# Kernel optimization log

Measured on AMD Instinct MI355X. Metric: run time of the kernel, lower is better.

The kernel has to match this reference:

```python
import jax, jax.numpy as jnp
import numpy as np
from jax import lax

NPOINT = 1024   # FPS centroids
NSAMPLE = 32    # neighbors per ball
RADIUS = 0.1    # ball-query radius (points live in unit cube)


def farthest_point_sample(pos, npoint):
    # pos: [B, N, 3] -> idx [B, npoint] int32
    B, N, _ = pos.shape

    def step(carry, _):
        min_d, far = carry                                   # [B,N], [B]
        centroid = jnp.take_along_axis(pos, far[:, None, None], axis=1)  # [B,1,3]
        d = jnp.sum((pos - centroid) ** 2, axis=-1)          # [B,N]
        min_d = jnp.minimum(min_d, d)
        nxt = jnp.argmax(min_d, axis=1).astype(jnp.int32)
        return (min_d, nxt), far

    init = (jnp.full((B, N), 1e10, pos.dtype), jnp.zeros((B,), jnp.int32))
    _, idx = lax.scan(step, init, None, length=npoint)
    return idx.T                                             # [B, npoint]


def ball_query(new_pos, pos, radius, k):
    # new_pos: [B,M,3], pos: [B,N,3] -> idx [B,M,k] int32
    d2 = (jnp.sum(new_pos ** 2, -1)[:, :, None]
          + jnp.sum(pos ** 2, -1)[:, None, :]
          - 2.0 * jnp.einsum('bmc,bnc->bmn', new_pos, pos))  # [B,M,N]
    neg = jnp.where(d2 <= radius * radius, -d2, -jnp.inf)
    vals, idx = lax.top_k(neg, k)                            # k nearest inside ball
    valid = vals > -jnp.inf
    idx = jnp.where(valid, idx, idx[..., :1])                # replicate first hit (centroid itself)
    return idx.astype(jnp.int32)


def setup_inputs() -> dict:
    key = jax.random.key(0)
    ks = jax.random.split(key, 6)
    B, N, C = 4, 16384, 1
    pos = jax.random.uniform(ks[0], (B, N, 3), dtype=jnp.float32)
    x = jax.random.normal(ks[1], (B, N, C), dtype=jnp.float32)
    c_in = 3 + C  # rel-xyz concat features
    W1 = jax.random.normal(ks[2], (c_in, 32), jnp.float32) * np.sqrt(2.0 / c_in)
    W2 = jax.random.normal(ks[3], (32, 32), jnp.float32) * np.sqrt(2.0 / 32)
    W3 = jax.random.normal(ks[4], (32, 32), jnp.float32) * np.sqrt(2.0 / 32)
    b1 = jnp.zeros((32,), jnp.float32)
    b2 = jnp.zeros((32,), jnp.float32)
    b3 = jnp.zeros((32,), jnp.float32)
    return {"pos": pos, "x": x, "W1": W1, "b1": b1, "W2": W2, "b2": b2, "W3": W3, "b3": b3}


def reference(pos, x, W1, b1, W2, b2, W3, b3):
    # PointNet++ set-abstraction: FPS -> ball query -> group -> shared MLP -> max-pool.
    fps_idx = farthest_point_sample(lax.stop_gradient(pos), NPOINT)       # [B,M]
    new_pos = jnp.take_along_axis(pos, fps_idx[..., None], axis=1)        # [B,M,3]
    idx = ball_query(lax.stop_gradient(new_pos), lax.stop_gradient(pos), RADIUS, NSAMPLE)  # [B,M,K]
    B, M, K = idx.shape
    flat = idx.reshape(B, M * K)
    gpos = jnp.take_along_axis(pos, flat[..., None], axis=1).reshape(B, M, K, 3)
    gx = jnp.take_along_axis(x, flat[..., None], axis=1).reshape(B, M, K, -1)
    rel = gpos - new_pos[:, :, None, :]                                   # local coords
    h = jnp.concatenate([rel, gx], axis=-1)                               # [B,M,K,4]
    h = jax.nn.relu(h @ W1 + b1)
    h = jax.nn.relu(h @ W2 + b2)
    h = jax.nn.relu(h @ W3 + b3)
    return jnp.max(h, axis=2)                                             # [B,M,32]
```

## Files before the change

kernel.cpp:

```cpp
#include <hip/hip_runtime.h>

#define NB 4
#define NPT 16384
#define NPOINT 1024
#define NSAMPLE 32

#define FPS_T 512
#define FPS_PPT (NPT / FPS_T)

#define BQ_WAVES 4
#define CAP 896

__global__ __launch_bounds__(FPS_T, 2) void fps_kernel(
    const float* __restrict__ pos, float* __restrict__ new_pos) {
#pragma clang fp contract(off)
  const int b = blockIdx.x;
  const int tid = threadIdx.x;
  const int wid = tid >> 6;
  const int lane = tid & 63;
  const float* __restrict__ p = pos + (size_t)b * NPT * 3;

  __shared__ float2 sxy[NPT];
  __shared__ unsigned long long red[3];

  float z[FPS_PPT], md[FPS_PPT];

  {
    const float4* pf4 = (const float4*)(p + (size_t)tid * (FPS_PPT * 3));
#pragma unroll
    for (int k = 0; k < FPS_PPT / 4; ++k) {
      const float4 a = pf4[3 * k + 0];
      const float4 bq = pf4[3 * k + 1];
      const float4 c = pf4[3 * k + 2];
      sxy[(4 * k + 0) * FPS_T + tid] = make_float2(a.x, a.y);
      z[4 * k + 0] = a.z;
      sxy[(4 * k + 1) * FPS_T + tid] = make_float2(a.w, bq.x);
      z[4 * k + 1] = bq.y;
      sxy[(4 * k + 2) * FPS_T + tid] = make_float2(bq.z, bq.w);
      z[4 * k + 2] = c.x;
      sxy[(4 * k + 3) * FPS_T + tid] = make_float2(c.y, c.z);
      z[4 * k + 3] = c.w;
    }
#pragma unroll
    for (int i = 0; i < FPS_PPT; ++i) md[i] = 1e10f;
  }

  if (tid < 3) red[tid] = 0ull;
  __syncthreads();

  float cx = p[0], cy = p[1], cz = p[2];

  for (int j = 0; j < NPOINT; ++j) {
    if (tid == 0) {
      float* q = new_pos + ((size_t)b * NPOINT + j) * 3;
      q[0] = cx;
      q[1] = cy;
      q[2] = cz;
    }
    float bm = -1.0f;
    int bi = 0;
#pragma unroll
    for (int i = 0; i < FPS_PPT; ++i) {
      const float2 xy = sxy[i * FPS_T + tid];
      const float dx = xy.x - cx;
      const float dy = xy.y - cy;
      const float dz = z[i] - cz;
      const float d = (dx * dx + dy * dy) + dz * dz;
      const float m = fminf(md[i], d);
      md[i] = m;
      if (m > bm) {
        bm = m;
        bi = i;
      }
    }
    float wm = bm;
#pragma unroll
    for (int off = 1; off < 64; off <<= 1)
      wm = fmaxf(wm, __shfl_xor(wm, off, 64));
    const unsigned long long tied = __ballot(bm == wm);
    const int wl = __ffsll((long long)tied) - 1;
    const int wbi = __shfl(bi, wl, 64);
    const int widx = ((wid << 6) + wl) * FPS_PPT + wbi;
    if (lane == 0) {
      const unsigned long long key =
          ((unsigned long long)__float_as_uint(wm) << 32) |
          (unsigned)(~widx);
      atomicMax(&red[j % 3], key);
    }
    __syncthreads();
    const unsigned long long w = red[j % 3];
    if (tid == 0) red[(j + 2) % 3] = 0ull;
    const int nf = (int)(~(unsigned)w);
    cx = p[nf * 3 + 0];
    cy = p[nf * 3 + 1];
    cz = p[nf * 3 + 2];
  }
}

__global__ __launch_bounds__(256) void bq_mlp_kernel(
    const float* __restrict__ pos, const float* __restrict__ x,
    const float* __restrict__ W1, const float* __restrict__ b1,
    const float* __restrict__ W2, const float* __restrict__ b2,
    const float* __restrict__ W3, const float* __restrict__ b3,
    const float* __restrict__ new_pos, float* __restrict__ out) {
#pragma clang fp contract(off)
  __shared__ __align__(16) float w1s[4 * 32];
  __shared__ __align__(16) float w2s[32 * 32];
  __shared__ __align__(16) float w3s[32 * 32];
  __shared__ float b1s[32], b2s[32], b3s[32];
  __shared__ unsigned long long list[BQ_WAVES][CAP];
  __shared__ int sel[BQ_WAVES][NSAMPLE];
  __shared__ unsigned cnt[BQ_WAVES];

  const int tid = threadIdx.x;
  const int wid = tid >> 6;
  const int lane = tid & 63;

  for (int i = tid; i < 128; i += 256) w1s[i] = W1[i];
  for (int i = tid; i < 1024; i += 256) {
    w2s[i] = W2[i];
    w3s[i] = W3[i];
  }
  if (tid < 32) {
    b1s[tid] = b1[tid];
    b2s[tid] = b2[tid];
    b3s[tid] = b3[tid];
  }
  if (lane == 0) cnt[wid] = 0u;
  __syncthreads();

  const int m_global = blockIdx.x * BQ_WAVES + wid;
  const int b = m_global >> 10;
  const float* __restrict__ p = pos + (size_t)b * NPT * 3;
  const float* __restrict__ xb = x + (size_t)b * NPT;

  const float cx = new_pos[(size_t)m_global * 3 + 0];
  const float cy = new_pos[(size_t)m_global * 3 + 1];
  const float cz = new_pos[(size_t)m_global * 3 + 2];
  const float snew = (cx * cx + cy * cy) + cz * cz;

  for (int it = 0; it < NPT / 256; ++it) {
    const int n0 = it * 256 + lane * 4;
    const float4* pf4 = (const float4*)(p + (size_t)n0 * 3);
    const float4 a = pf4[0];
    const float4 bq = pf4[1];
    const float4 c = pf4[2];
    float qx[4], qy[4], qz[4];
    qx[0] = a.x;  qy[0] = a.y;  qz[0] = a.z;
    qx[1] = a.w;  qy[1] = bq.x; qz[1] = bq.y;
    qx[2] = bq.z; qy[2] = bq.w; qz[2] = c.x;
    qx[3] = c.y;  qy[3] = c.z;  qz[3] = c.w;
#pragma unroll
    for (int t = 0; t < 4; ++t) {
      const float spos = (qx[t] * qx[t] + qy[t] * qy[t]) + qz[t] * qz[t];
      const float dot = (cx * qx[t] + cy * qy[t]) + cz * qz[t];
      const float d2 = (snew + spos) - 2.0f * dot;
      if (d2 <= 0.01f) {
        const unsigned u = __float_as_uint(d2);
        const unsigned key = (u & 0x80000000u) ? ~u : (u | 0x80000000u);
        const unsigned li = atomicAdd(&cnt[wid], 1u);
        if (li < CAP)
          list[wid][li] = ((unsigned long long)key << 32) | (unsigned)(n0 + t);
      }
    }
  }
  __syncthreads();

  int c = (int)cnt[wid];
  if (c > CAP) c = CAP;
  const int nsel = c < NSAMPLE ? c : NSAMPLE;

  for (int i = lane; i < c; i += 64) {
    const unsigned long long ki = list[wid][i];
    int rank = 0;
    for (int jj = 0; jj < c; ++jj) rank += (list[wid][jj] < ki) ? 1 : 0;
    if (rank < NSAMPLE) sel[wid][rank] = (int)(unsigned)(ki & 0xFFFFFFFFull);
  }
  __syncthreads();

  const bool active = (lane < nsel);
  const int n = sel[wid][active ? lane : 0];

  const float gpx = p[n * 3 + 0];
  const float gpy = p[n * 3 + 1];
  const float gpz = p[n * 3 + 2];
  const float gxv = xb[n];

  const float h0 = gpx - cx, h1i = gpy - cy, h2i = gpz - cz, h3i = gxv;

  float h1[32];
#pragma unroll
  for (int o = 0; o < 32; ++o) {
    float a = b1s[o];
    a += h0 * w1s[0 * 32 + o];
    a += h1i * w1s[1 * 32 + o];
    a += h2i * w1s[2 * 32 + o];
    a += h3i * w1s[3 * 32 + o];
    h1[o] = fmaxf(a, 0.0f);
  }

  float acc[32];
#pragma unroll
  for (int o = 0; o < 32; ++o) acc[o] = b2s[o];
  for (int k = 0; k < 32; ++k) {
    const float hk = h1[k];
    const float4* row = (const float4*)&w2s[k * 32];
#pragma unroll
    for (int q = 0; q < 8; ++q) {
      const float4 ww = row[q];
      acc[4 * q + 0] += hk * ww.x;
      acc[4 * q + 1] += hk * ww.y;
      acc[4 * q + 2] += hk * ww.z;
      acc[4 * q + 3] += hk * ww.w;
    }
  }
#pragma unroll
  for (int o = 0; o < 32; ++o) h1[o] = fmaxf(acc[o], 0.0f);

#pragma unroll
  for (int o = 0; o < 32; ++o) acc[o] = b3s[o];
  for (int k = 0; k < 32; ++k) {
    const float hk = h1[k];
    const float4* row = (const float4*)&w3s[k * 32];
#pragma unroll
    for (int q = 0; q < 8; ++q) {
      const float4 ww = row[q];
      acc[4 * q + 0] += hk * ww.x;
      acc[4 * q + 1] += hk * ww.y;
      acc[4 * q + 2] += hk * ww.z;
      acc[4 * q + 3] += hk * ww.w;
    }
  }
#pragma unroll
  for (int o = 0; o < 32; ++o)
    acc[o] = active ? fmaxf(acc[o], 0.0f) : -INFINITY;

#pragma unroll
  for (int mask = 1; mask <= 16; mask <<= 1) {
#pragma unroll
    for (int o = 0; o < 32; ++o)
      acc[o] = fmaxf(acc[o], __shfl_xor(acc[o], mask, 64));
  }

  if (lane == 0) {
    float4* o4 = (float4*)(out + (size_t)m_global * 32);
#pragma unroll
    for (int q = 0; q < 8; ++q)
      o4[q] = make_float4(acc[4 * q + 0], acc[4 * q + 1], acc[4 * q + 2],
                          acc[4 * q + 3]);
  }
}

extern "C" void kernel_launch(void* const* d_in, const int* in_sizes, int n_in,
                              void* d_out, int out_size, void* d_ws,
                              size_t ws_size, hipStream_t stream) {
  const float* pos = (const float*)d_in[0];
  const float* x = (const float*)d_in[1];
  const float* W1 = (const float*)d_in[2];
  const float* b1 = (const float*)d_in[3];
  const float* W2 = (const float*)d_in[4];
  const float* b2 = (const float*)d_in[5];
  const float* W3 = (const float*)d_in[6];
  const float* b3 = (const float*)d_in[7];
  float* out = (float*)d_out;
  float* new_pos = (float*)d_ws;

  fps_kernel<<<NB, FPS_T, 0, stream>>>(pos, new_pos);
  bq_mlp_kernel<<<(NB * NPOINT) / BQ_WAVES, 256, 0, stream>>>(
      pos, x, W1, b1, W2, b2, W3, b3, new_pos, out);
}
```

Measured before the change: 1.940 ms.

## Speed up FPS loop with DPP reduction, float4 LDS, and on-chip centroid fetch

The FPS inner loop now reads xy pairs for two points per LDS load by packing them into float4. The wave max uses DPP row/broadcast steps plus readlane instead of a shfl_xor butterfly. The next centroid is read from LDS, with z taken from a per-wave winner slot, instead of a dependent global load after the barrier. The new_pos write is also rotated across threads so it no longer always lands on thread 0. All of this shortens the serial per-iteration critical path, at the cost of relying on the index encoding and on DPP semantics being correct.

Measured after the change: 1.939 ms. Within noise of the previous version (-0.0%).

```diff
diff --git a/kernel.cpp b/kernel.cpp
--- a/kernel.cpp
+++ b/kernel.cpp
@@ -10,6 +10,13 @@
 
 #define BQ_WAVES 4
 #define CAP 896
+
+template <int CTRL>
+__device__ __forceinline__ float dpp_max_step(float v) {
+  const int s =
+      __builtin_amdgcn_update_dpp(0, __float_as_int(v), CTRL, 0xf, 0xf, true);
+  return fmaxf(v, __int_as_float(s));
+}
 
 __global__ __launch_bounds__(FPS_T, 2) void fps_kernel(
     const float* __restrict__ pos, float* __restrict__ new_pos) {
@@ -20,8 +27,9 @@
   const int lane = tid & 63;
   const float* __restrict__ p = pos + (size_t)b * NPT * 3;
 
-  __shared__ float2 sxy[NPT];
+  __shared__ float4 sxy4[NPT / 2];
   __shared__ unsigned long long red[3];
+  __shared__ float wzs[3][8];
 
   float z[FPS_PPT], md[FPS_PPT];
 
@@ -32,13 +40,11 @@
       const float4 a = pf4[3 * k + 0];
       const float4 bq = pf4[3 * k + 1];
       const float4 c = pf4[3 * k + 2];
-      sxy[(4 * k + 0) * FPS_T + tid] = make_float2(a.x, a.y);
+      sxy4[(2 * k + 0) * FPS_T + tid] = make_float4(a.x, a.y, a.w, bq.x);
+      sxy4[(2 * k + 1) * FPS_T + tid] = make_float4(bq.z, bq.w, c.y, c.z);
       z[4 * k + 0] = a.z;
-      sxy[(4 * k + 1) * FPS_T + tid] = make_float2(a.w, bq.x);
       z[4 * k + 1] = bq.y;
-      sxy[(4 * k + 2) * FPS_T + tid] = make_float2(bq.z, bq.w);
       z[4 * k + 2] = c.x;
-      sxy[(4 * k + 3) * FPS_T + tid] = make_float2(c.y, c.z);
       z[4 * k + 3] = c.w;
     }
 #pragma unroll
@@ -51,7 +57,7 @@
   float cx = p[0], cy = p[1], cz = p[2];
 
   for (int j = 0; j < NPOINT; ++j) {
-    if (tid == 0) {
+    if (tid == (((j & 7) << 6) | ((j >> 3) & 63))) {
       float* q = new_pos + ((size_t)b * NPOINT + j) * 3;
       q[0] = cx;
       q[1] = cy;
@@ -59,41 +65,71 @@
     }
     float bm = -1.0f;
     int bi = 0;
-#pragma unroll
-    for (int i = 0; i < FPS_PPT; ++i) {
-      const float2 xy = sxy[i * FPS_T + tid];
-      const float dx = xy.x - cx;
-      const float dy = xy.y - cy;
-      const float dz = z[i] - cz;
-      const float d = (dx * dx + dy * dy) + dz * dz;
-      const float m = fminf(md[i], d);
-      md[i] = m;
-      if (m > bm) {
-        bm = m;
-        bi = i;
+    float bz = 0.0f;
+#pragma unroll
+    for (int i2 = 0; i2 < FPS_PPT / 2; ++i2) {
+      const float4 q4 = sxy4[i2 * FPS_T + tid];
+      {
+        const int i = 2 * i2;
+        const float dx = q4.x - cx;
+        const float dy = q4.y - cy;
+        const float dz = z[i] - cz;
+        const float d = (dx * dx + dy * dy) + dz * dz;
+        const float m = fminf(md[i], d);
+        md[i] = m;
+        if (m > bm) {
+          bm = m;
+          bi = i;
+          bz = z[i];
+        }
       }
-    }
-    float wm = bm;
-#pragma unroll
-    for (int off = 1; off < 64; off <<= 1)
-      wm = fmaxf(wm, __shfl_xor(wm, off, 64));
+      {
+        const int i = 2 * i2 + 1;
+        const float dx = q4.z - cx;
+        const float dy = q4.w - cy;
+        const float dz = z[i] - cz;
+        const float d = (dx * dx + dy * dy) + dz * dz;
+        const float m = fminf(md[i], d);
+        md[i] = m;
+        if (m > bm) {
+          bm = m;
+          bi = i;
+          bz = z[i];
+        }
+      }
+    }
+    float v = bm;
+    v = dpp_max_step<0x111>(v);
+    v = dpp_max_step<0x112>(v);
+    v = dpp_max_step<0x114>(v);
+    v = dpp_max_step<0x118>(v);
+    v = dpp_max_step<0x142>(v);
+    v = dpp_max_step<0x143>(v);
+    const float wm =
+        __int_as_float(__builtin_amdgcn_readlane(__float_as_int(v), 63));
     const unsigned long long tied = __ballot(bm == wm);
     const int wl = __ffsll((long long)tied) - 1;
-    const int wbi = __shfl(bi, wl, 64);
+    const int wbi = __builtin_amdgcn_readlane(bi, wl);
+    const float wbz =
+        __int_as_float(__builtin_amdgcn_readlane(__float_as_int(bz), wl));
     const int widx = ((wid << 6) + wl) * FPS_PPT + wbi;
     if (lane == 0) {
       const unsigned long long key =
           ((unsigned long long)__float_as_uint(wm) << 32) |
           (unsigned)(~widx);
       atomicMax(&red[j % 3], key);
+      wzs[j % 3][wid] = wbz;
     }
     __syncthreads();
     const unsigned long long w = red[j % 3];
     if (tid == 0) red[(j + 2) % 3] = 0ull;
     const int nf = (int)(~(unsigned)w);
-    cx = p[nf * 3 + 0];
-    cy = p[nf * 3 + 1];
-    cz = p[nf * 3 + 2];
+    cz = wzs[j % 3][nf >> 11];
+    const int ot = nf >> 5;
+    const int oi = nf & 31;
+    const float4 q4 = sxy4[(oi >> 1) * FPS_T + ot];
+    cx = (oi & 1) ? q4.z : q4.x;
+    cy = (oi & 1) ? q4.w : q4.y;
   }
 }
 
```
